# Performance work log

Measured on AMD Instinct MI355X. Metric: run time of the kernel, lower is better.

The kernel has to match this reference:

```python
import jax, jax.numpy as jnp
import numpy as np

B, L, H, E = 4, 2048, 8, 64
WINDOW = 8
DILATION = 1


def setup_inputs() -> dict:
    key = jax.random.key(0)
    kq, kk, kv, ka = jax.random.split(key, 4)
    queries = jax.random.normal(kq, (B, L, H, E), dtype=jnp.float32)
    keys = jax.random.normal(kk, (B, L, H, E), dtype=jnp.float32)
    values = jax.random.normal(kv, (B, L, H, E), dtype=jnp.float32)
    alpha = jax.random.uniform(ka, (1,), dtype=jnp.float32)
    return {"queries": queries, "keys": keys, "values": values, "alpha": alpha}


def _full_attention(q, k, v, scale):
    # q,k,v: [B, L, H, E]
    scores = jnp.einsum('blhe,bshe->bhls', q, k) * scale  # [B,H,L,L]
    A = jax.nn.softmax(scores, axis=-1)
    return jnp.einsum('bhls,bshd->blhd', A, v)


def _local_attention(q, k, v, scale):
    # efficient gather-based local window attention, non-causal
    Lk = k.shape[1]
    offsets = jnp.arange(-WINDOW, WINDOW + 1) * DILATION
    idx = jnp.clip(jnp.arange(Lk)[:, None] + offsets[None, :], 0, Lk - 1)
    K_win = k[:, idx]
    V_win = v[:, idx]
    scores = jnp.einsum('blhe,blwhe->blhw', q, K_win) * scale
    A = jax.nn.softmax(scores, axis=-1)
    return jnp.einsum('blhw,blwhe->blhe', A, V_win)


def reference(queries, keys, values, alpha):
    scale = 1.0 / np.sqrt(queries.shape[-1]).astype(np.float32)
    out_full = _full_attention(queries, keys, values, scale)
    out_local = _local_attention(queries, keys, values, scale)
    w = jax.nn.sigmoid(alpha[0])
    # only_target_first=True: positions 1..L-1 take out_full, position 0 is gated
    out = out_full.at[:, 0].set(w * out_full[:, 0] + (1.0 - w) * out_local[:, 0])
    return out
```

## Files before the change

kernel.cpp:

```cpp
#include <hip/hip_runtime.h>

typedef unsigned short u16;
typedef unsigned int   u32;
typedef __attribute__((ext_vector_type(8))) short short8;
typedef __attribute__((ext_vector_type(4))) float f32x4;

#define MFMA16(a, b, c) __builtin_amdgcn_mfma_f32_16x16x32_bf16(a, b, c, 0, 0, 0)

constexpr int Lv = 2048, Hv = 8, Ev = 64, HE = Hv * Ev;
constexpr float QSCALE = 0.18033688011112042f;

__device__ __forceinline__ float bf2f(u16 u) {
    u32 x = ((u32)u) << 16;
    return __builtin_bit_cast(float, x);
}
__device__ __forceinline__ u16 f2bf(float f) {
    u32 x = __builtin_bit_cast(u32, f);
    u32 r = ((x >> 16) & 1u) + 0x7fffu;
    return (u16)((x + r) >> 16);
}
__device__ __forceinline__ u32 pkbf(float a, float b) {
#if __has_builtin(__builtin_amdgcn_cvt_pk_bf16_f32)
    typedef __attribute__((ext_vector_type(2))) __bf16 bf16x2;
    bf16x2 v = __builtin_amdgcn_cvt_pk_bf16_f32(a, b);
    return __builtin_bit_cast(u32, v);
#else
    return (u32)f2bf(a) | ((u32)f2bf(b) << 16);
#endif
}
__device__ __forceinline__ float fexp2(float x) {
#if __has_builtin(__builtin_amdgcn_exp2f)
    return __builtin_amdgcn_exp2f(x);
#else
    return exp2f(x);
#endif
}

__device__ __forceinline__ int detect_isbf16(const u32* q32, int lane) {
    u32 w0 = q32[2 * lane];
    u32 w1 = q32[2 * lane + 1];
    u16 uu[4] = { (u16)(w0 & 0xffff), (u16)(w0 >> 16),
                  (u16)(w1 & 0xffff), (u16)(w1 >> 16) };
    int p = 0, z = 0;
#pragma unroll
    for (int j = 0; j < 4; ++j) {
        u16 mgn = (u16)(uu[j] & 0x7fff);
        int ex  = mgn >> 7;
        bool zero = (mgn == 0);
        bool pl   = zero || (ex >= 115 && ex <= 132);
        p += pl ? 1 : 0;
        if ((j & 1) == 0) z += zero ? 1 : 0;
    }
    int acc = p | (z << 16);
#pragma unroll
    for (int o = 1; o < 64; o <<= 1) acc += __shfl_xor(acc, o);
    int ps = acc & 0xffff, zs = acc >> 16;
    if (zs >= 100) return 0;
    return (ps >= 240) ? 1 : 0;
}

__device__ __forceinline__ short8 cvt8s(const float* p, float s) {
    float4 a = *(const float4*)p, b4 = *(const float4*)(p + 4);
    u32 r[4] = { pkbf(a.x * s, a.y * s), pkbf(a.z * s, a.w * s),
                 pkbf(b4.x * s, b4.y * s), pkbf(b4.z * s, b4.w * s) };
    return *(short8*)r;
}

template <int ISBF>
__device__ __forceinline__ void attn_impl(
    const void* __restrict__ qv, const void* __restrict__ kv,
    const void* __restrict__ vv, const void* __restrict__ alphav,
    void* __restrict__ outv, u16* Klds, u16* Vt, u16* PldsAll)
{
    const int tid  = threadIdx.x;
    const int w    = tid >> 6;
    const int lane = tid & 63;
    const int quad = lane >> 4;
    const int m    = lane & 15;

    const int fid = blockIdx.x;
    const int bh  = (fid & 7) * 4 + ((fid >> 3) & 3);
    const int rb  = fid >> 5;
    const int b   = bh >> 3, h = bh & 7;
    const int row0 = rb * 128;

    const size_t bhoff = (size_t)b * Lv * HE + h * Ev;
    const u16*   q16 = (const u16*)qv + bhoff;
    const u16*   k16 = (const u16*)kv + bhoff;
    const u16*   v16 = (const u16*)vv + bhoff;
    const float* q32 = (const float*)qv + bhoff;
    const float* k32 = (const float*)kv + bhoff;
    const float* v32 = (const float*)vv + bhoff;

    short8 qf[2][2];
#pragma unroll
    for (int mt = 0; mt < 2; ++mt) {
        size_t ro = (size_t)(row0 + w * 32 + mt * 16 + m) * HE + quad * 8;
        if (ISBF) {
            short8 t0 = *(const short8*)(q16 + ro);
            short8 t1 = *(const short8*)(q16 + ro + 32);
#pragma unroll
            for (int j = 0; j < 8; ++j) {
                qf[mt][0][j] = (short)f2bf(bf2f((u16)t0[j]) * QSCALE);
                qf[mt][1][j] = (short)f2bf(bf2f((u16)t1[j]) * QSCALE);
            }
        } else {
            qf[mt][0] = cvt8s(q32 + ro, QSCALE);
            qf[mt][1] = cvt8s(q32 + ro + 32, QSCALE);
        }
    }

    short8 ones8;
#pragma unroll
    for (int j = 0; j < 8; ++j) ones8[j] = (short)0x3F80;

    f32x4 O[2][4];
    f32x4 Ssum[2];
#pragma unroll
    for (int mt = 0; mt < 2; ++mt) {
        Ssum[mt] = f32x4{0.f, 0.f, 0.f, 0.f};
#pragma unroll
        for (int et = 0; et < 4; ++et) O[mt][et] = f32x4{0.f, 0.f, 0.f, 0.f};
    }

    int koff[2];
#pragma unroll
    for (int t = 0; t < 2; ++t) {
        int ci  = tid + t * 256;
        int key = ci >> 3, sl = ci & 7;
        koff[t] = key * HE + (sl ^ (key & 7)) * 8;
    }
    const int eq = tid & 15;
    const int ppu[2] = { tid >> 4, (tid >> 4) + 16 };

    u16* Pw = PldsAll + w * 2048;

    uint4  kr[2];  uint2  vr[2][2];
    float4 kf[2][2]; float4 vf[2][2];

    auto load_tile = [&](int KT) {
        if (ISBF) {
#pragma unroll
            for (int t = 0; t < 2; ++t)
                kr[t] = *(const uint4*)(k16 + (size_t)KT * 64 * HE + koff[t]);
#pragma unroll
            for (int u = 0; u < 2; ++u) {
                const u16* vp = v16 + (size_t)(KT * 64 + 2 * ppu[u]) * HE + eq * 4;
                vr[u][0] = *(const uint2*)vp;
                vr[u][1] = *(const uint2*)(vp + HE);
            }
        } else {
#pragma unroll
            for (int t = 0; t < 2; ++t) {
                const float* kp = k32 + (size_t)KT * 64 * HE + koff[t];
                kf[t][0] = *(const float4*)kp;
                kf[t][1] = *(const float4*)(kp + 4);
            }
#pragma unroll
            for (int u = 0; u < 2; ++u) {
                const float* vp = v32 + (size_t)(KT * 64 + 2 * ppu[u]) * HE + eq * 4;
                vf[u][0] = *(const float4*)vp;
                vf[u][1] = *(const float4*)(vp + HE);
            }
        }
    };
    auto store_tile = [&](u16* KB, u16* VB) {
        if (ISBF) {
#pragma unroll
            for (int t = 0; t < 2; ++t)
                *(uint4*)&KB[(tid + t * 256) * 8] = kr[t];
#pragma unroll
            for (int u = 0; u < 2; ++u) {
                int pp = ppu[u], kcv = pp >> 2, pq = pp & 3;
                const u16* a0 = (const u16*)&vr[u][0];
                const u16* a1 = (const u16*)&vr[u][1];
#pragma unroll
                for (int j = 0; j < 4; ++j) {
                    int e  = eq * 4 + j;
                    int sl = kcv ^ ((e + (e >> 3)) & 7);
                    u32 val = (u32)a0[j] | ((u32)a1[j] << 16);
                    *(u32*)&VB[e * 64 + sl * 8 + pq * 2] = val;
                }
            }
        } else {
#pragma unroll
            for (int t = 0; t < 2; ++t) {
                u32 kk[4] = { pkbf(kf[t][0].x, kf[t][0].y), pkbf(kf[t][0].z, kf[t][0].w),
                              pkbf(kf[t][1].x, kf[t][1].y), pkbf(kf[t][1].z, kf[t][1].w) };
                *(uint4*)&KB[(tid + t * 256) * 8] = *(uint4*)kk;
            }
#pragma unroll
            for (int u = 0; u < 2; ++u) {
                int pp = ppu[u], kcv = pp >> 2, pq = pp & 3;
                float t0[4], t1[4];
                *(float4*)t0 = vf[u][0];
                *(float4*)t1 = vf[u][1];
#pragma unroll
                for (int j = 0; j < 4; ++j) {
                    int e  = eq * 4 + j;
                    int sl = kcv ^ ((e + (e >> 3)) & 7);
                    *(u32*)&VB[e * 64 + sl * 8 + pq * 2] = pkbf(t0[j], t1[j]);
                }
            }
        }
    };

    load_tile(0);
    store_tile(Klds, Vt);
    __syncthreads();

    for (int kt = 0; kt < 32; ++kt) {
        u16* Kb = Klds + (kt & 1) * 4096;
        u16* Vb = Vt   + (kt & 1) * 4096;
        u16* Kn = Klds + ((kt & 1) ^ 1) * 4096;
        u16* Vn = Vt   + ((kt & 1) ^ 1) * 4096;

        if (kt < 31) load_tile(kt + 1);

        f32x4 St[2][4];
#pragma unroll
        for (int mt = 0; mt < 2; ++mt)
#pragma unroll
            for (int nt = 0; nt < 4; ++nt) St[mt][nt] = f32x4{0.f, 0.f, 0.f, 0.f};
#pragma unroll
        for (int c = 0; c < 2; ++c) {
#pragma unroll
            for (int nt = 0; nt < 4; ++nt) {
                int krow = nt * 16 + m;
                int sl   = (4 * c + quad) ^ (m & 7);
                short8 kfr = *(const short8*)&Kb[krow * 64 + sl * 8];
                St[0][nt] = MFMA16(kfr, qf[0][c], St[0][nt]);
                St[1][nt] = MFMA16(kfr, qf[1][c], St[1][nt]);
            }
        }

#pragma unroll
        for (int mt = 0; mt < 2; ++mt) {
#pragma unroll
            for (int nt = 0; nt < 4; ++nt) {
                u32 u0 = pkbf(fexp2(St[mt][nt][0]), fexp2(St[mt][nt][1]));
                u32 u1 = pkbf(fexp2(St[mt][nt][2]), fexp2(St[mt][nt][3]));
                int G   = 2 * nt + (quad >> 1);
                int off = (mt * 16 + m) * 64 + ((G ^ (m & 7)) * 8) + (quad & 1) * 4;
                uint2 val; val.x = u0; val.y = u1;
                *(uint2*)&Pw[off] = val;
            }
        }

#pragma unroll
        for (int c = 0; c < 2; ++c) {
            int Gp = (4 * c + quad) ^ (m & 7);
            short8 pf0 = *(const short8*)&Pw[m * 64 + Gp * 8];
            short8 pf1 = *(const short8*)&Pw[(16 + m) * 64 + Gp * 8];
            Ssum[0] = MFMA16(pf0, ones8, Ssum[0]);
            Ssum[1] = MFMA16(pf1, ones8, Ssum[1]);
#pragma unroll
            for (int et = 0; et < 4; ++et) {
                int e  = et * 16 + m;
                int sl = (4 * c + quad) ^ ((e + (e >> 3)) & 7);
                short8 vfr = *(const short8*)&Vb[e * 64 + sl * 8];
                O[0][et] = MFMA16(pf0, vfr, O[0][et]);
                O[1][et] = MFMA16(pf1, vfr, O[1][et]);
            }
        }

        if (kt < 31) {
            store_tile(Kn, Vn);
            __syncthreads();
        }
    }

    float locv[4] = {0.f, 0.f, 0.f, 0.f};
    float wgt = 0.f;
    const bool isrow0 = (rb == 0) && (w == 0) && (quad == 0);
    if (rb == 0 && w == 0) {
        const int e = lane;
        const size_t base = bhoff + e;
#define LDIN(p, i) (ISBF ? bf2f(((const u16*)(p))[i]) : ((const float*)(p))[i])
        float qe = LDIN(qv, base);
        float s[9];
#pragma unroll
        for (int j = 0; j < 9; ++j) {
            float prod = qe * LDIN(kv, base + (size_t)j * HE);
#pragma unroll
            for (int o = 1; o < 64; o <<= 1) prod += __shfl_xor(prod, o);
            s[j] = prod * 0.125f;
        }
        float mx = s[0];
#pragma unroll
        for (int j = 1; j < 9; ++j) mx = fmaxf(mx, s[j]);
        float we[9];
#pragma unroll
        for (int j = 0; j < 9; ++j) we[j] = expf(s[j] - mx);
        float denom = 9.f * we[0];
        float acc   = 9.f * we[0] * LDIN(vv, base);
#pragma unroll
        for (int j = 1; j < 9; ++j) {
            denom += we[j];
            acc   += we[j] * LDIN(vv, base + (size_t)j * HE);
        }
        float loc = acc / denom;

        float a;
        if (ISBF) {
            a = bf2f(((const u16*)alphav)[0]);
            if (!(a >= 0.0f && a <= 1.0f)) {
                float af = ((const float*)alphav)[0];
                if (af >= 0.0f && af <= 1.0f) a = af;
            }
        } else {
            a = ((const float*)alphav)[0];
            if (!(a >= 0.0f && a <= 1.0f)) {
                float ab = bf2f(((const u16*)alphav)[0]);
                if (ab >= 0.0f && ab <= 1.0f) a = ab;
            }
        }
        wgt = 1.f / (1.f + expf(-a));
#pragma unroll
        for (int et = 0; et < 4; ++et) locv[et] = __shfl(loc, et * 16 + m);
#undef LDIN
    }

#pragma unroll
    for (int mt = 0; mt < 2; ++mt) {
#pragma unroll
        for (int r = 0; r < 4; ++r) {
            float inv = 1.0f / Ssum[mt][r];
            int row = row0 + w * 32 + mt * 16 + quad * 4 + r;
            size_t oo = (size_t)(b * Lv + row) * HE + h * Ev + m;
            bool blend = isrow0 && (mt == 0) && (r == 0);
#pragma unroll
            for (int et = 0; et < 4; ++et) {
                float res = O[mt][et][r] * inv;
                if (blend) res = wgt * res + (1.f - wgt) * locv[et];
                if (ISBF) ((u16*)outv)[oo + et * 16] = f2bf(res);
                else      ((float*)outv)[oo + et * 16] = res;
            }
        }
    }
}

__global__ __launch_bounds__(256, 2) void attn_kernel(
    const void* __restrict__ qv, const void* __restrict__ kv,
    const void* __restrict__ vv, const void* __restrict__ alphav,
    void* __restrict__ outv)
{
    __shared__ u16 Klds[2 * 64 * 64];
    __shared__ u16 Vt[2 * 64 * 64];
    __shared__ u16 Plds[4 * 32 * 64];

    const int isbf = detect_isbf16((const u32*)qv, threadIdx.x & 63);
    if (isbf) attn_impl<1>(qv, kv, vv, alphav, outv, Klds, Vt, Plds);
    else      attn_impl<0>(qv, kv, vv, alphav, outv, Klds, Vt, Plds);
}

extern "C" void kernel_launch(void* const* d_in, const int* in_sizes, int n_in,
                              void* d_out, int out_size, void* d_ws, size_t ws_size,
                              hipStream_t stream) {
    hipLaunchKernelGGL(attn_kernel, dim3(512), dim3(256), 0, stream,
                       d_in[0], d_in[1], d_in[2], d_in[3], d_out);
}
```

Baseline: 148.2 us.

## Split key tiles across two wave groups with LDS reduction of partial outputs

Doubles the block to 512 threads. Two groups of four waves each own the same query rows and process alternate 64-key tiles (even or odd), and at the end the second group's partial O and row sums go through LDS to be added into the first group's accumulators. Each thread now loads one K/V chunk per tile instead of two, and the aim is more waves per CU to hide latency and MFMA dependencies. The cost is a final LDS reduction, extra barriers, and half the waves sitting idle at each tile step between the shared syncs.

```diff
diff --git a/kernel.cpp b/kernel.cpp
--- a/kernel.cpp
+++ b/kernel.cpp
@@ -70,10 +70,12 @@
 __device__ __forceinline__ void attn_impl(
     const void* __restrict__ qv, const void* __restrict__ kv,
     const void* __restrict__ vv, const void* __restrict__ alphav,
-    void* __restrict__ outv, u16* Klds, u16* Vt, u16* PldsAll)
+    void* __restrict__ outv, u16* Klds, u16* Vt, u16* PldsAll, float* Scmb)
 {
     const int tid  = threadIdx.x;
     const int w    = tid >> 6;
+    const int g    = w & 3;
+    const int par  = w >> 2;
     const int lane = tid & 63;
     const int quad = lane >> 4;
     const int m    = lane & 15;
@@ -95,7 +97,7 @@
     short8 qf[2][2];
 #pragma unroll
     for (int mt = 0; mt < 2; ++mt) {
-        size_t ro = (size_t)(row0 + w * 32 + mt * 16 + m) * HE + quad * 8;
+        size_t ro = (size_t)(row0 + g * 32 + mt * 16 + m) * HE + quad * 8;
         if (ISBF) {
             short8 t0 = *(const short8*)(q16 + ro);
             short8 t1 = *(const short8*)(q16 + ro + 32);
@@ -123,84 +125,54 @@
         for (int et = 0; et < 4; ++et) O[mt][et] = f32x4{0.f, 0.f, 0.f, 0.f};
     }
 
-    int koff[2];
-#pragma unroll
-    for (int t = 0; t < 2; ++t) {
-        int ci  = tid + t * 256;
-        int key = ci >> 3, sl = ci & 7;
-        koff[t] = key * HE + (sl ^ (key & 7)) * 8;
-    }
-    const int eq = tid & 15;
-    const int ppu[2] = { tid >> 4, (tid >> 4) + 16 };
+    const int kkey = tid >> 3, ksl = tid & 7;
+    const int koff = kkey * HE + (ksl ^ (kkey & 7)) * 8;
+    const int eq = tid & 15, pp = tid >> 4;
+    const int kcv = pp >> 2, pq = pp & 3;
 
     u16* Pw = PldsAll + w * 2048;
 
-    uint4  kr[2];  uint2  vr[2][2];
-    float4 kf[2][2]; float4 vf[2][2];
+    uint4 kru; uint2 vru0, vru1;
+    float4 kfa, kfb, vfa, vfb;
 
     auto load_tile = [&](int KT) {
         if (ISBF) {
-#pragma unroll
-            for (int t = 0; t < 2; ++t)
-                kr[t] = *(const uint4*)(k16 + (size_t)KT * 64 * HE + koff[t]);
-#pragma unroll
-            for (int u = 0; u < 2; ++u) {
-                const u16* vp = v16 + (size_t)(KT * 64 + 2 * ppu[u]) * HE + eq * 4;
-                vr[u][0] = *(const uint2*)vp;
-                vr[u][1] = *(const uint2*)(vp + HE);
-            }
+            kru  = *(const uint4*)(k16 + (size_t)KT * 64 * HE + koff);
+            const u16* vp = v16 + (size_t)(KT * 64 + 2 * pp) * HE + eq * 4;
+            vru0 = *(const uint2*)vp;
+            vru1 = *(const uint2*)(vp + HE);
         } else {
-#pragma unroll
-            for (int t = 0; t < 2; ++t) {
-                const float* kp = k32 + (size_t)KT * 64 * HE + koff[t];
-                kf[t][0] = *(const float4*)kp;
-                kf[t][1] = *(const float4*)(kp + 4);
-            }
-#pragma unroll
-            for (int u = 0; u < 2; ++u) {
-                const float* vp = v32 + (size_t)(KT * 64 + 2 * ppu[u]) * HE + eq * 4;
-                vf[u][0] = *(const float4*)vp;
-                vf[u][1] = *(const float4*)(vp + HE);
-            }
+            const float* kp = k32 + (size_t)KT * 64 * HE + koff;
+            kfa = *(const float4*)kp;
+            kfb = *(const float4*)(kp + 4);
+            const float* vp = v32 + (size_t)(KT * 64 + 2 * pp) * HE + eq * 4;
+            vfa = *(const float4*)vp;
+            vfb = *(const float4*)(vp + HE);
         }
     };
     auto store_tile = [&](u16* KB, u16* VB) {
         if (ISBF) {
-#pragma unroll
-            for (int t = 0; t < 2; ++t)
-                *(uint4*)&KB[(tid + t * 256) * 8] = kr[t];
-#pragma unroll
-            for (int u = 0; u < 2; ++u) {
-                int pp = ppu[u], kcv = pp >> 2, pq = pp & 3;
-                const u16* a0 = (const u16*)&vr[u][0];
-                const u16* a1 = (const u16*)&vr[u][1];
-#pragma unroll
-                for (int j = 0; j < 4; ++j) {
-                    int e  = eq * 4 + j;
-                    int sl = kcv ^ ((e + (e >> 3)) & 7);
-                    u32 val = (u32)a0[j] | ((u32)a1[j] << 16);
-                    *(u32*)&VB[e * 64 + sl * 8 + pq * 2] = val;
-                }
+            *(uint4*)&KB[tid * 8] = kru;
+            const u16* a0 = (const u16*)&vru0;
+            const u16* a1 = (const u16*)&vru1;
+#pragma unroll
+            for (int j = 0; j < 4; ++j) {
+                int e  = eq * 4 + j;
+                int sl = kcv ^ ((e + (e >> 3)) & 7);
+                u32 val = (u32)a0[j] | ((u32)a1[j] << 16);
+                *(u32*)&VB[e * 64 + sl * 8 + pq * 2] = val;
             }
         } else {
-#pragma unroll
-            for (int t = 0; t < 2; ++t) {
-                u32 kk[4] = { pkbf(kf[t][0].x, kf[t][0].y), pkbf(kf[t][0].z, kf[t][0].w),
-                              pkbf(kf[t][1].x, kf[t][1].y), pkbf(kf[t][1].z, kf[t][1].w) };
-                *(uint4*)&KB[(tid + t * 256) * 8] = *(uint4*)kk;
-            }
-#pragma unroll
-            for (int u = 0; u < 2; ++u) {
-                int pp = ppu[u], kcv = pp >> 2, pq = pp & 3;
-                float t0[4], t1[4];
-                *(float4*)t0 = vf[u][0];
-                *(float4*)t1 = vf[u][1];
-#pragma unroll
-                for (int j = 0; j < 4; ++j) {
-                    int e  = eq * 4 + j;
-                    int sl = kcv ^ ((e + (e >> 3)) & 7);
-                    *(u32*)&VB[e * 64 + sl * 8 + pq * 2] = pkbf(t0[j], t1[j]);
-                }
+            u32 kk[4] = { pkbf(kfa.x, kfa.y), pkbf(kfa.z, kfa.w),
+                          pkbf(kfb.x, kfb.y), pkbf(kfb.z, kfb.w) };
+            *(uint4*)&KB[tid * 8] = *(uint4*)kk;
+            float t0[4], t1[4];
+            *(float4*)t0 = vfa; *(float4*)t1 = vfb;
+#pragma unroll
+            for (int j = 0; j < 4; ++j) {
+                int e  = eq * 4 + j;
+                int sl = kcv ^ ((e + (e >> 3)) & 7);
+                *(u32*)&VB[e * 64 + sl * 8 + pq * 2] = pkbf(t0[j], t1[j]);
             }
         }
     };
@@ -217,50 +189,52 @@
 
         if (kt < 31) load_tile(kt + 1);
 
-        f32x4 St[2][4];
-#pragma unroll
-        for (int mt = 0; mt < 2; ++mt)
-#pragma unroll
-            for (int nt = 0; nt < 4; ++nt) St[mt][nt] = f32x4{0.f, 0.f, 0.f, 0.f};
-#pragma unroll
-        for (int c = 0; c < 2; ++c) {
-#pragma unroll
-            for (int nt = 0; nt < 4; ++nt) {
-                int krow = nt * 16 + m;
-                int sl   = (4 * c + quad) ^ (m & 7);
-                short8 kfr = *(const short8*)&Kb[krow * 64 + sl * 8];
-                St[0][nt] = MFMA16(kfr, qf[0][c], St[0][nt]);
-                St[1][nt] = MFMA16(kfr, qf[1][c], St[1][nt]);
-            }
-        }
-
-#pragma unroll
-        for (int mt = 0; mt < 2; ++mt) {
-#pragma unroll
-            for (int nt = 0; nt < 4; ++nt) {
-                u32 u0 = pkbf(fexp2(St[mt][nt][0]), fexp2(St[mt][nt][1]));
-                u32 u1 = pkbf(fexp2(St[mt][nt][2]), fexp2(St[mt][nt][3]));
-                int G   = 2 * nt + (quad >> 1);
-                int off = (mt * 16 + m) * 64 + ((G ^ (m & 7)) * 8) + (quad & 1) * 4;
-                uint2 val; val.x = u0; val.y = u1;
-                *(uint2*)&Pw[off] = val;
-            }
-        }
-
-#pragma unroll
-        for (int c = 0; c < 2; ++c) {
-            int Gp = (4 * c + quad) ^ (m & 7);
-            short8 pf0 = *(const short8*)&Pw[m * 64 + Gp * 8];
-            short8 pf1 = *(const short8*)&Pw[(16 + m) * 64 + Gp * 8];
-            Ssum[0] = MFMA16(pf0, ones8, Ssum[0]);
-            Ssum[1] = MFMA16(pf1, ones8, Ssum[1]);
-#pragma unroll
-            for (int et = 0; et < 4; ++et) {
-                int e  = et * 16 + m;
-                int sl = (4 * c + quad) ^ ((e + (e >> 3)) & 7);
-                short8 vfr = *(const short8*)&Vb[e * 64 + sl * 8];
-                O[0][et] = MFMA16(pf0, vfr, O[0][et]);
-                O[1][et] = MFMA16(pf1, vfr, O[1][et]);
+        if ((kt & 1) == par) {
+            f32x4 St[2][4];
+#pragma unroll
+            for (int mt = 0; mt < 2; ++mt)
+#pragma unroll
+                for (int nt = 0; nt < 4; ++nt) St[mt][nt] = f32x4{0.f,0.f,0.f,0.f};
+#pragma unroll
+            for (int c = 0; c < 2; ++c) {
+#pragma unroll
+                for (int nt = 0; nt < 4; ++nt) {
+                    int krow = nt * 16 + m;
+                    int sl   = (4 * c + quad) ^ (m & 7);
+                    short8 kfr = *(const short8*)&Kb[krow * 64 + sl * 8];
+                    St[0][nt] = MFMA16(kfr, qf[0][c], St[0][nt]);
+                    St[1][nt] = MFMA16(kfr, qf[1][c], St[1][nt]);
+                }
+            }
+
+#pragma unroll
+            for (int mt = 0; mt < 2; ++mt) {
+#pragma unroll
+                for (int nt = 0; nt < 4; ++nt) {
+                    u32 u0 = pkbf(fexp2(St[mt][nt][0]), fexp2(St[mt][nt][1]));
+                    u32 u1 = pkbf(fexp2(St[mt][nt][2]), fexp2(St[mt][nt][3]));
+                    int G   = 2 * nt + (quad >> 1);
+                    int off = (mt * 16 + m) * 64 + ((G ^ (m & 7)) * 8) + (quad & 1) * 4;
+                    uint2 val; val.x = u0; val.y = u1;
+                    *(uint2*)&Pw[off] = val;
+                }
+            }
+
+#pragma unroll
+            for (int c = 0; c < 2; ++c) {
+                int Gp = (4 * c + quad) ^ (m & 7);
+                short8 pf0 = *(const short8*)&Pw[m * 64 + Gp * 8];
+                short8 pf1 = *(const short8*)&Pw[(16 + m) * 64 + Gp * 8];
+                Ssum[0] = MFMA16(pf0, ones8, Ssum[0]);
+                Ssum[1] = MFMA16(pf1, ones8, Ssum[1]);
+#pragma unroll
+                for (int et = 0; et < 4; ++et) {
+                    int e  = et * 16 + m;
+                    int sl = (4 * c + quad) ^ ((e + (e >> 3)) & 7);
+                    short8 vfr = *(const short8*)&Vb[e * 64 + sl * 8];
+                    O[0][et] = MFMA16(pf0, vfr, O[0][et]);
+                    O[1][et] = MFMA16(pf1, vfr, O[1][et]);
+                }
             }
         }
 
@@ -269,6 +243,24 @@
             __syncthreads();
         }
     }
+
+    __syncthreads();
+    if (w >= 4) {
+        float* ob = (float*)PldsAll + (size_t)(w - 4) * 2048;
+        float* sb = Scmb + (w - 4) * 512;
+#pragma unroll
+        for (int mt = 0; mt < 2; ++mt) {
+#pragma unroll
+            for (int et = 0; et < 4; ++et)
+#pragma unroll
+                for (int r = 0; r < 4; ++r)
+                    ob[(mt * 16 + et * 4 + r) * 64 + lane] = O[mt][et][r];
+#pragma unroll
+            for (int r = 0; r < 4; ++r)
+                sb[(mt * 4 + r) * 64 + lane] = Ssum[mt][r];
+        }
+    }
+    __syncthreads();
 
     float locv[4] = {0.f, 0.f, 0.f, 0.f};
     float wgt = 0.f;
@@ -321,42 +313,58 @@
 #undef LDIN
     }
 
-#pragma unroll
-    for (int mt = 0; mt < 2; ++mt) {
-#pragma unroll
-        for (int r = 0; r < 4; ++r) {
-            float inv = 1.0f / Ssum[mt][r];
-            int row = row0 + w * 32 + mt * 16 + quad * 4 + r;
-            size_t oo = (size_t)(b * Lv + row) * HE + h * Ev + m;
-            bool blend = isrow0 && (mt == 0) && (r == 0);
-#pragma unroll
-            for (int et = 0; et < 4; ++et) {
-                float res = O[mt][et][r] * inv;
-                if (blend) res = wgt * res + (1.f - wgt) * locv[et];
-                if (ISBF) ((u16*)outv)[oo + et * 16] = f2bf(res);
-                else      ((float*)outv)[oo + et * 16] = res;
-            }
-        }
-    }
-}
-
-__global__ __launch_bounds__(256, 2) void attn_kernel(
+    if (w < 4) {
+        const float* ob = (const float*)PldsAll + (size_t)w * 2048;
+        const float* sb = Scmb + w * 512;
+#pragma unroll
+        for (int mt = 0; mt < 2; ++mt) {
+#pragma unroll
+            for (int r = 0; r < 4; ++r)
+                Ssum[mt][r] += sb[(mt * 4 + r) * 64 + lane];
+#pragma unroll
+            for (int et = 0; et < 4; ++et)
+#pragma unroll
+                for (int r = 0; r < 4; ++r)
+                    O[mt][et][r] += ob[(mt * 16 + et * 4 + r) * 64 + lane];
+        }
+#pragma unroll
+        for (int mt = 0; mt < 2; ++mt) {
+#pragma unroll
+            for (int r = 0; r < 4; ++r) {
+                float inv = 1.0f / Ssum[mt][r];
+                int row = row0 + g * 32 + mt * 16 + quad * 4 + r;
+                size_t oo = (size_t)(b * Lv + row) * HE + h * Ev + m;
+                bool blend = isrow0 && (mt == 0) && (r == 0);
+#pragma unroll
+                for (int et = 0; et < 4; ++et) {
+                    float res = O[mt][et][r] * inv;
+                    if (blend) res = wgt * res + (1.f - wgt) * locv[et];
+                    if (ISBF) ((u16*)outv)[oo + et * 16] = f2bf(res);
+                    else      ((float*)outv)[oo + et * 16] = res;
+                }
+            }
+        }
+    }
+}
+
+__global__ __launch_bounds__(512, 4) void attn_kernel(
     const void* __restrict__ qv, const void* __restrict__ kv,
     const void* __restrict__ vv, const void* __restrict__ alphav,
     void* __restrict__ outv)
 {
-    __shared__ u16 Klds[2 * 64 * 64];
-    __shared__ u16 Vt[2 * 64 * 64];
-    __shared__ u16 Plds[4 * 32 * 64];
+    __shared__ u16 Klds[2 * 4096];
+    __shared__ u16 Vt[2 * 4096];
+    __shared__ u16 Plds[8 * 2048];
+    __shared__ float Scmb[4 * 512];
 
     const int isbf = detect_isbf16((const u32*)qv, threadIdx.x & 63);
-    if (isbf) attn_impl<1>(qv, kv, vv, alphav, outv, Klds, Vt, Plds);
-    else      attn_impl<0>(qv, kv, vv, alphav, outv, Klds, Vt, Plds);
+    if (isbf) attn_impl<1>(qv, kv, vv, alphav, outv, Klds, Vt, Plds, Scmb);
+    else      attn_impl<0>(qv, kv, vv, alphav, outv, Klds, Vt, Plds, Scmb);
 }
 
 extern "C" void kernel_launch(void* const* d_in, const int* in_sizes, int n_in,
                               void* d_out, int out_size, void* d_ws, size_t ws_size,
                               hipStream_t stream) {
-    hipLaunchKernelGGL(attn_kernel, dim3(512), dim3(256), 0, stream,
+    hipLaunchKernelGGL(attn_kernel, dim3(512), dim3(512), 0, stream,
                        d_in[0], d_in[1], d_in[2], d_in[3], d_out);
 }
```

After: 282.8 us. 90.9% more time.
